# Kernel tuning notes

Hardware: AMD Instinct MI355X
Metric: run time of the kernel (lower is better)

## Reference

```python
import jax, jax.numpy as jnp
import numpy as np

B, Q, K, QSIZE, KSIZE, H, VDIM = 4, 1024, 1024, 256, 256, 32, 256


def setup_inputs() -> dict:
    key = jax.random.key(0)
    ks = jax.random.split(key, 10)
    return {
        "keys": jax.random.normal(ks[0], (B, K, KSIZE), dtype=jnp.float32),
        "queries": jax.random.normal(ks[1], (B, Q, QSIZE), dtype=jnp.float32),
        "values": jax.random.normal(ks[2], (B, K, VDIM), dtype=jnp.float32),
        "valid_lens": jax.random.randint(ks[3], (B,), 1, K + 1, dtype=jnp.int32),
        "W_q": jax.random.normal(ks[4], (QSIZE, H), dtype=jnp.float32) * (QSIZE ** -0.5),
        "b_q": jnp.zeros((H,), dtype=jnp.float32),
        "W_k": jax.random.normal(ks[5], (KSIZE, H), dtype=jnp.float32) * (KSIZE ** -0.5),
        "b_k": jnp.zeros((H,), dtype=jnp.float32),
        "w_v": jax.random.normal(ks[6], (H,), dtype=jnp.float32) * (H ** -0.5),
        "b_v": jnp.zeros((), dtype=jnp.float32),
    }


def reference(keys, queries, values, valid_lens, W_q, b_q, W_k, b_k, w_v, b_v):
    # projected features: (B,K,H) and (B,Q,H)
    fk = keys @ W_k + b_k
    fq = queries @ W_q + b_q
    # broadcast add -> (B,Q,K,H), tanh, then scalar projection -> scores (B,Q,K)
    features = jnp.tanh(fq[:, :, None, :] + fk[:, None, :, :])
    scores = jnp.einsum("bqkh,h->bqk", features, w_v) + b_v
    # masked softmax over key axis: positions >= valid_len get -1e6
    mask = jnp.arange(K)[None, None, :] < valid_lens[:, None, None]
    scores = jnp.where(mask, scores, jnp.float32(-1e6))
    weights = jax.nn.softmax(scores, axis=-1)
    # bmm: (B,Q,K) @ (B,K,V) -> (B,Q,V)
    return jnp.einsum("bqk,bkv->bqv", weights, values)
```

## Files before the change

### kernel.cpp

```cpp
#include <hip/hip_runtime.h>
#include <math.h>


#define NB 4
#define NQ 1024
#define NK 1024
#define DQK 256
#define NH 32
#define NV 256
#define TQ 16
#define BLK 1024

typedef __attribute__((ext_vector_type(2))) float f32x2;

__device__ __forceinline__ float fast_rcp(float x) { return __builtin_amdgcn_rcpf(x); }

__global__ __launch_bounds__(256) void proj_kernel(
    const float* __restrict__ queries, const float* __restrict__ keys,
    const float* __restrict__ W_q, const float* __restrict__ b_q,
    const float* __restrict__ W_k, const float* __restrict__ b_k,
    float* __restrict__ eq, float* __restrict__ ek)
{
    const int tid     = blockIdx.x * 256 + threadIdx.x;
    const int g       = tid >> 5;
    const int sub     = tid & 31;
    const int h4      = (sub & 7) * 4;
    const int quarter = sub >> 3;

    const int row0 = g * 2;
    const float* src; const float* W; const float* bias; float* dst; int r;
    if (row0 < NB * NQ) { r = row0;           src = queries + (size_t)r * DQK; W = W_q; bias = b_q; dst = eq; }
    else                { r = row0 - NB * NQ; src = keys    + (size_t)r * DQK; W = W_k; bias = b_k; dst = ek; }

    f32x2 a01A = {0.f, 0.f}, a23A = {0.f, 0.f};
    f32x2 a01B = {0.f, 0.f}, a23B = {0.f, 0.f};
    if (quarter == 0) {
        float4 bv4 = *(const float4*)(bias + h4);
        a01A = (f32x2){bv4.x, bv4.y}; a23A = (f32x2){bv4.z, bv4.w};
        a01B = a01A; a23B = a23A;
    }
    const float* srcA = src;
    const float* srcB = src + DQK;
    const int d0 = quarter * 64;
    #pragma unroll 4
    for (int i = d0; i < d0 + 64; i += 4) {
        float4 sA = *(const float4*)(srcA + i);
        float4 sB = *(const float4*)(srcB + i);
        float4 w0 = *(const float4*)(W + (size_t)(i + 0) * NH + h4);
        float4 w1 = *(const float4*)(W + (size_t)(i + 1) * NH + h4);
        float4 w2 = *(const float4*)(W + (size_t)(i + 2) * NH + h4);
        float4 w3 = *(const float4*)(W + (size_t)(i + 3) * NH + h4);
#define PSTEP2(SA, SB, WR) \
        a01A = __builtin_elementwise_fma((f32x2){SA, SA}, (f32x2){WR.x, WR.y}, a01A); \
        a23A = __builtin_elementwise_fma((f32x2){SA, SA}, (f32x2){WR.z, WR.w}, a23A); \
        a01B = __builtin_elementwise_fma((f32x2){SB, SB}, (f32x2){WR.x, WR.y}, a01B); \
        a23B = __builtin_elementwise_fma((f32x2){SB, SB}, (f32x2){WR.z, WR.w}, a23B);
        PSTEP2(sA.x, sB.x, w0) PSTEP2(sA.y, sB.y, w1)
        PSTEP2(sA.z, sB.z, w2) PSTEP2(sA.w, sB.w, w3)
#undef PSTEP2
    }
    float a0A = a01A.x, a1A = a01A.y, a2A = a23A.x, a3A = a23A.y;
    float a0B = a01B.x, a1B = a01B.y, a2B = a23B.x, a3B = a23B.y;
    a0A += __shfl_xor(a0A, 8, 64);  a1A += __shfl_xor(a1A, 8, 64);
    a2A += __shfl_xor(a2A, 8, 64);  a3A += __shfl_xor(a3A, 8, 64);
    a0B += __shfl_xor(a0B, 8, 64);  a1B += __shfl_xor(a1B, 8, 64);
    a2B += __shfl_xor(a2B, 8, 64);  a3B += __shfl_xor(a3B, 8, 64);
    a0A += __shfl_xor(a0A, 16, 64); a1A += __shfl_xor(a1A, 16, 64);
    a2A += __shfl_xor(a2A, 16, 64); a3A += __shfl_xor(a3A, 16, 64);
    a0B += __shfl_xor(a0B, 16, 64); a1B += __shfl_xor(a1B, 16, 64);
    a2B += __shfl_xor(a2B, 16, 64); a3B += __shfl_xor(a3B, 16, 64);
    if (quarter == 0) {
        float4 oA, oB;
        oA.x = __expf(2.f * a0A); oA.y = __expf(2.f * a1A);
        oA.z = __expf(2.f * a2A); oA.w = __expf(2.f * a3A);
        oB.x = __expf(2.f * a0B); oB.y = __expf(2.f * a1B);
        oB.z = __expf(2.f * a2B); oB.w = __expf(2.f * a3B);
        *(float4*)(dst + (size_t)r * NH + h4)       = oA;
        *(float4*)(dst + (size_t)(r + 1) * NH + h4) = oB;
    }
}

__global__ __launch_bounds__(BLK, 4) void attn_kernel(
    const float* __restrict__ eq, const float* __restrict__ ek,
    const float* __restrict__ values, const int* __restrict__ valid_lens,
    const float* __restrict__ w_v, float* __restrict__ out)
{
    __shared__ float sred_buf[8 * TQ * 256];
    __shared__ float s_part[16][TQ];
    float (*s_w)[TQ] = (float (*)[TQ])sred_buf;

    const int t      = threadIdx.x;
    const int b      = blockIdx.x >> 6;
    const int q0     = (blockIdx.x & 63) * TQ;
    const int nvalid = valid_lens[b];
    const int wave   = t >> 6;
    const int lane   = t & 63;
    const int qi     = lane & 15;
    const int kk     = lane >> 4;

    const int kpw  = (nvalid + 15) >> 4;
    const int kbeg = wave * kpw;
    const int kend = min(nvalid, kbeg + kpw);

    float wv[NH];
    #pragma unroll
    for (int h = 0; h < NH; h += 4) {
        float4 w4 = *(const float4*)(w_v + h);
        wv[h] = w4.x; wv[h+1] = w4.y; wv[h+2] = w4.z; wv[h+3] = w4.w;
    }
    float eqr[NH];
    const float* eqp = eq + (size_t)(b * NQ + q0 + qi) * NH;
    #pragma unroll
    for (int h = 0; h < NH; h += 4) {
        float4 e4 = *(const float4*)(eqp + h);
        eqr[h] = e4.x; eqr[h+1] = e4.y; eqr[h+2] = e4.z; eqr[h+3] = e4.w;
    }

    const float* ekbase = ek + (size_t)b * NK * NH;
    float ssum = 0.f;
    for (int k0 = kbeg; k0 < kend; k0 += 4) {
        const int k = k0 + kk;
        if (k < kend) {
            const float* ekp = ekbase + (size_t)k * NH;
            float acc = 0.f;
            #pragma unroll
            for (int h = 0; h < NH; h += 4) {
                float4 e4 = *(const float4*)(ekp + h);
                float u0 = fmaf(eqr[h+0], e4.x, 1.f);
                float u1 = fmaf(eqr[h+1], e4.y, 1.f);
                float u2 = fmaf(eqr[h+2], e4.z, 1.f);
                float u3 = fmaf(eqr[h+3], e4.w, 1.f);
                float d01 = u0 * u1, d23 = u2 * u3;
                float n01 = fmaf(wv[h+0], u1, wv[h+1] * u0);
                float n23 = fmaf(wv[h+2], u3, wv[h+3] * u2);
                float d   = fminf(d01 * d23, 1e38f);
                float n   = fmaf(n01, d23, n23 * d01);
                acc = fmaf(n, fast_rcp(d), acc);
            }
            float e = __expf(-2.f * acc);
            s_w[k][qi] = e;
            ssum += e;
        }
    }

    ssum += __shfl_xor(ssum, 16, 64);
    ssum += __shfl_xor(ssum, 32, 64);
    if (lane < TQ) s_part[wave][lane] = ssum;

    f32x2 al[TQ], ah[TQ];
    #pragma unroll
    for (int j = 0; j < TQ; j++) { al[j] = (f32x2){0.f, 0.f}; ah[j] = (f32x2){0.f, 0.f}; }
    const float* vbase = values + (size_t)b * NK * NV + 4 * lane;

    #pragma unroll 2
    for (int k = kbeg; k < kend; k++) {
        float4 v  = *(const float4*)(vbase + (size_t)k * NV);
        f32x2 vl = {v.x, v.y}, vh = {v.z, v.w};
        float4 w0 = *(const float4*)(&s_w[k][0]);
        float4 w1 = *(const float4*)(&s_w[k][4]);
        float4 w2 = *(const float4*)(&s_w[k][8]);
        float4 w3 = *(const float4*)(&s_w[k][12]);
        const float wq[TQ] = {w0.x,w0.y,w0.z,w0.w, w1.x,w1.y,w1.z,w1.w,
                              w2.x,w2.y,w2.z,w2.w, w3.x,w3.y,w3.z,w3.w};
        #pragma unroll
        for (int j = 0; j < TQ; j++) {
            al[j] = __builtin_elementwise_fma((f32x2){wq[j], wq[j]}, vl, al[j]);
            ah[j] = __builtin_elementwise_fma((f32x2){wq[j], wq[j]}, vh, ah[j]);
        }
    }

    __syncthreads();
    float* sred = sred_buf;
    float4* p = (float4*)(sred + (size_t)((wave & 7) * TQ) * 256) + lane;
    if (wave < 8) {
        #pragma unroll
        for (int j = 0; j < TQ; j++)
            p[j * 64] = (float4){al[j].x, al[j].y, ah[j].x, ah[j].y};
    }
    __syncthreads();
    if (wave >= 8) {
        #pragma unroll
        for (int j = 0; j < TQ; j++) {
            float4 x4 = p[j * 64];
            x4.x += al[j].x; x4.y += al[j].y; x4.z += ah[j].x; x4.w += ah[j].y;
            p[j * 64] = x4;
        }
    }
    __syncthreads();

    const int v  = t & 255;
    const int qh = (t >> 8) * 4;
    float* obase = out + (size_t)(b * NQ + q0) * NV + v;
    #pragma unroll
    for (int jj = 0; jj < 4; jj++) {
        const int q = qh + jj;
        float tot = 0.f;
        #pragma unroll
        for (int w = 0; w < 16; w++) tot += s_part[w][q];
        float rs = fast_rcp(tot);
        float r = 0.f;
        #pragma unroll
        for (int reg = 0; reg < 8; reg++) r += sred[(size_t)(reg * TQ + q) * 256 + v];
        obase[(size_t)q * NV] = r * rs;
    }
}

extern "C" void kernel_launch(void* const* d_in, const int* in_sizes, int n_in,
                              void* d_out, int out_size, void* d_ws, size_t ws_size,
                              hipStream_t stream) {
    (void)in_sizes; (void)n_in; (void)out_size; (void)ws_size;
    const float* keys       = (const float*)d_in[0];
    const float* queries    = (const float*)d_in[1];
    const float* values     = (const float*)d_in[2];
    const int*   valid_lens = (const int*)d_in[3];
    const float* W_q        = (const float*)d_in[4];
    const float* b_q        = (const float*)d_in[5];
    const float* W_k        = (const float*)d_in[6];
    const float* b_k        = (const float*)d_in[7];
    const float* w_v        = (const float*)d_in[8];
    float* out = (float*)d_out;

    float* eq = (float*)d_ws;
    float* ek = eq + (size_t)NB * NQ * NH;

    proj_kernel<<<dim3(512), dim3(256), 0, stream>>>(queries, keys, W_q, b_q, W_k, b_k, eq, ek);
    attn_kernel<<<dim3(NB * (NQ / TQ)), dim3(BLK), 0, stream>>>(eq, ek, values, valid_lens, w_v, out);
}
```

Before: 115.6 us.

## Split key range across two blocks and combine partial sums in a third kernel

New measurement: 110.5 us. 4.4% less time.

```diff
diff --git a/kernel.cpp b/kernel.cpp
--- a/kernel.cpp
+++ b/kernel.cpp
@@ -9,7 +9,7 @@
 #define NH 32
 #define NV 256
 #define TQ 16
-#define BLK 1024
+#define BLK 512
 
 typedef __attribute__((ext_vector_type(2))) float f32x2;
 
@@ -83,24 +83,31 @@
 __global__ __launch_bounds__(BLK, 4) void attn_kernel(
     const float* __restrict__ eq, const float* __restrict__ ek,
     const float* __restrict__ values, const int* __restrict__ valid_lens,
-    const float* __restrict__ w_v, float* __restrict__ out)
+    const float* __restrict__ w_v, float* __restrict__ num, float* __restrict__ den)
 {
-    __shared__ float sred_buf[8 * TQ * 256];
-    __shared__ float s_part[16][TQ];
-    float (*s_w)[TQ] = (float (*)[TQ])sred_buf;
+    __shared__ float sbuf[4 * TQ * 256];
+    __shared__ float s_part[8][TQ];
+    float (*s_w)[TQ] = (float (*)[TQ])sbuf;
 
     const int t      = threadIdx.x;
-    const int b      = blockIdx.x >> 6;
-    const int q0     = (blockIdx.x & 63) * TQ;
+    const int b      = blockIdx.x >> 7;
+    const int qg     = (blockIdx.x >> 1) & 63;
+    const int kh     = blockIdx.x & 1;
+    const int q0     = qg * TQ;
     const int nvalid = valid_lens[b];
     const int wave   = t >> 6;
     const int lane   = t & 63;
     const int qi     = lane & 15;
     const int kk     = lane >> 4;
 
-    const int kpw  = (nvalid + 15) >> 4;
-    const int kbeg = wave * kpw;
-    const int kend = min(nvalid, kbeg + kpw);
+    const int half_len = (nvalid + 1) >> 1;
+    const int k_lo  = kh * half_len;
+    const int k_hi  = min(nvalid, k_lo + half_len);
+    const int count = k_hi - k_lo;
+
+    const int kpw  = (count + 7) >> 3;
+    const int kbeg = k_lo + wave * kpw;
+    const int kend = min(k_hi, kbeg + kpw);
 
     float wv[NH];
     #pragma unroll
@@ -138,7 +145,7 @@
                 acc = fmaf(n, fast_rcp(d), acc);
             }
             float e = __expf(-2.f * acc);
-            s_w[k][qi] = e;
+            s_w[k - k_lo][qi] = e;
             ssum += e;
         }
     }
@@ -156,10 +163,11 @@
     for (int k = kbeg; k < kend; k++) {
         float4 v  = *(const float4*)(vbase + (size_t)k * NV);
         f32x2 vl = {v.x, v.y}, vh = {v.z, v.w};
-        float4 w0 = *(const float4*)(&s_w[k][0]);
-        float4 w1 = *(const float4*)(&s_w[k][4]);
-        float4 w2 = *(const float4*)(&s_w[k][8]);
-        float4 w3 = *(const float4*)(&s_w[k][12]);
+        const int kl = k - k_lo;
+        float4 w0 = *(const float4*)(&s_w[kl][0]);
+        float4 w1 = *(const float4*)(&s_w[kl][4]);
+        float4 w2 = *(const float4*)(&s_w[kl][8]);
+        float4 w3 = *(const float4*)(&s_w[kl][12]);
         const float wq[TQ] = {w0.x,w0.y,w0.z,w0.w, w1.x,w1.y,w1.z,w1.w,
                               w2.x,w2.y,w2.z,w2.w, w3.x,w3.y,w3.z,w3.w};
         #pragma unroll
@@ -170,15 +178,14 @@
     }
 
     __syncthreads();
-    float* sred = sred_buf;
-    float4* p = (float4*)(sred + (size_t)((wave & 7) * TQ) * 256) + lane;
-    if (wave < 8) {
+    float4* p = (float4*)(sbuf + (size_t)((wave & 3) * TQ) * 256) + lane;
+    if (wave < 4) {
         #pragma unroll
         for (int j = 0; j < TQ; j++)
             p[j * 64] = (float4){al[j].x, al[j].y, ah[j].x, ah[j].y};
     }
     __syncthreads();
-    if (wave >= 8) {
+    if (wave >= 4) {
         #pragma unroll
         for (int j = 0; j < TQ; j++) {
             float4 x4 = p[j * 64];
@@ -189,20 +196,36 @@
     __syncthreads();
 
     const int v  = t & 255;
-    const int qh = (t >> 8) * 4;
-    float* obase = out + (size_t)(b * NQ + q0) * NV + v;
-    #pragma unroll
-    for (int jj = 0; jj < 4; jj++) {
+    const int qh = (t >> 8) * 8;
+    #pragma unroll
+    for (int jj = 0; jj < 8; jj++) {
         const int q = qh + jj;
+        float r = sbuf[(0*TQ + q) * 256 + v] + sbuf[(1*TQ + q) * 256 + v]
+                + sbuf[(2*TQ + q) * 256 + v] + sbuf[(3*TQ + q) * 256 + v];
+        num[(((size_t)(b * NQ + q0 + q) * 2) + kh) * NV + v] = r;
+    }
+    if (t < TQ) {
         float tot = 0.f;
         #pragma unroll
-        for (int w = 0; w < 16; w++) tot += s_part[w][q];
-        float rs = fast_rcp(tot);
-        float r = 0.f;
-        #pragma unroll
-        for (int reg = 0; reg < 8; reg++) r += sred[(size_t)(reg * TQ + q) * 256 + v];
-        obase[(size_t)q * NV] = r * rs;
-    }
+        for (int w = 0; w < 8; w++) tot += s_part[w][t];
+        den[((size_t)(b * NQ + q0 + t) * 2) + kh] = tot;
+    }
+}
+
+__global__ __launch_bounds__(256) void combine_kernel(
+    const float* __restrict__ num, const float* __restrict__ den,
+    float* __restrict__ out)
+{
+    const int g   = blockIdx.x * 256 + threadIdx.x;
+    const int row = g >> 6;
+    const int v4  = g & 63;
+    const float4* n4 = (const float4*)num;
+    float d = den[row * 2 + 0] + den[row * 2 + 1];
+    float4 a = n4[(size_t)(row * 2 + 0) * 64 + v4];
+    float4 c = n4[(size_t)(row * 2 + 1) * 64 + v4];
+    float rs = fast_rcp(d);
+    float4 o = {(a.x + c.x) * rs, (a.y + c.y) * rs, (a.z + c.z) * rs, (a.w + c.w) * rs};
+    ((float4*)out)[(size_t)row * 64 + v4] = o;
 }
 
 extern "C" void kernel_launch(void* const* d_in, const int* in_sizes, int n_in,
@@ -220,9 +243,12 @@
     const float* w_v        = (const float*)d_in[8];
     float* out = (float*)d_out;
 
-    float* eq = (float*)d_ws;
-    float* ek = eq + (size_t)NB * NQ * NH;
+    float* eq  = (float*)d_ws;
+    float* ek  = eq + (size_t)NB * NQ * NH;
+    float* num = ek + (size_t)NB * NK * NH;
+    float* den = num + (size_t)NB * NQ * 2 * NV;
 
     proj_kernel<<<dim3(512), dim3(256), 0, stream>>>(queries, keys, W_q, b_q, W_k, b_k, eq, ek);
-    attn_kernel<<<dim3(NB * (NQ / TQ)), dim3(BLK), 0, stream>>>(eq, ek, values, valid_lens, w_v, out);
-}
+    attn_kernel<<<dim3(NB * (NQ / TQ) * 2), dim3(BLK), 0, stream>>>(eq, ek, values, valid_lens, w_v, num, den);
+    combine_kernel<<<dim3(1024), dim3(256), 0, stream>>>(num, den, out);
+}
```
